# Performance work log

Measured on AMD Instinct MI355X. Metric: run time of the kernel, lower is better.

Reference implementation:

```python
import jax, jax.numpy as jnp
import numpy as np
import math

H, D = 8, 16
O = H * D  # out_channels = 128
N_TYPES = 2
EDGE_META = [(0, 1), (1, 0)]  # (src_type, dst_type) per edge type: user->item, item->user

def _segment_softmax(alpha, dst, n):
    # PyG softmax over incoming edges grouped by destination node
    amax = jax.ops.segment_max(alpha, dst, num_segments=n)
    amax = jnp.where(jnp.isfinite(amax), amax, 0.0)
    ex = jnp.exp(alpha - amax[dst])
    den = jax.ops.segment_sum(ex, dst, num_segments=n)
    return ex / (den[dst] + 1e-16)

def setup_inputs():
    key = jax.random.key(0)
    ks = jax.random.split(key, 8)
    N, E, I = 50000, 500000, 128
    s = 1.0 / math.sqrt(I)
    sd = 1.0 / math.sqrt(D)
    return {
        "x": jax.random.normal(ks[0], (N_TYPES, N, I), jnp.float32),
        "k_w": jax.random.normal(ks[1], (N_TYPES, O, I), jnp.float32) * s,
        "k_b": jnp.zeros((N_TYPES, O), jnp.float32),
        "q_w": jax.random.normal(ks[2], (N_TYPES, O, I), jnp.float32) * s,
        "q_b": jnp.zeros((N_TYPES, O), jnp.float32),
        "v_w": jax.random.normal(ks[3], (N_TYPES, O, I), jnp.float32) * s,
        "v_b": jnp.zeros((N_TYPES, O), jnp.float32),
        "a_w": jax.random.normal(ks[4], (N_TYPES, O, O), jnp.float32) * s,
        "a_b": jnp.zeros((N_TYPES, O), jnp.float32),
        "skip": jnp.ones((N_TYPES,), jnp.float32),
        "a_rel": jax.random.normal(ks[5], (2, H, D, D), jnp.float32) * sd,
        "m_rel": jax.random.normal(ks[6], (2, H, D, D), jnp.float32) * sd,
        "p_rel": jnp.ones((2, H), jnp.float32),
        "ln_g": jnp.ones((O,), jnp.float32),
        "ln_b": jnp.zeros((O,), jnp.float32),
        "edge_index": jax.random.randint(ks[7], (2, 2, E), 0, N, jnp.int32),
    }

def reference(x, k_w, k_b, q_w, q_b, v_w, v_b, a_w, a_b, skip, a_rel, m_rel, p_rel, ln_g, ln_b, edge_index):
    N = x.shape[1]
    lin = lambda xi, w, b: xi @ w.T + b
    # per-node-type K/Q/V projections -> [T, N, H, D]
    k = jnp.stack([lin(x[t], k_w[t], k_b[t]) for t in range(N_TYPES)]).reshape(N_TYPES, N, H, D)
    q = jnp.stack([lin(x[t], q_w[t], q_b[t]) for t in range(N_TYPES)]).reshape(N_TYPES, N, H, D)
    v = jnp.stack([lin(x[t], v_w[t], v_b[t]) for t in range(N_TYPES)]).reshape(N_TYPES, N, H, D)
    agg = jnp.zeros((N_TYPES, N, O), x.dtype)
    for e, (st, dt) in enumerate(EDGE_META):
        src, dst = edge_index[e, 0], edge_index[e, 1]
        ke = jnp.einsum('nhd,hde->nhe', k[st], a_rel[e])  # relation-transformed keys
        ve = jnp.einsum('nhd,hde->nhe', v[st], m_rel[e])  # relation-transformed values
        alpha = jnp.einsum('ehd,ehd->eh', q[dt][dst], ke[src]) * p_rel[e] / math.sqrt(D)
        alpha = _segment_softmax(alpha, dst, N)  # [E, H]
        msg = (ve[src] * alpha[..., None]).reshape(-1, O)
        agg = agg.at[dt].add(jax.ops.segment_sum(msg, dst, num_segments=N))
    outs = []
    for t in range(N_TYPES):
        o = lin(jax.nn.gelu(agg[t], approximate=False), a_w[t], a_b[t])
        beta = jax.nn.sigmoid(skip[t])
        o = beta * o + (1.0 - beta) * x[t]  # HGT skip (out_channels == in_channels)
        o = jax.nn.relu(o)
        mu = jnp.mean(o, axis=-1, keepdims=True)
        var = jnp.mean((o - mu) ** 2, axis=-1, keepdims=True)
        o = (o - mu) / jnp.sqrt(var + 1e-5) * ln_g + ln_b  # LayerNorm; dropout = identity (eval)
        outs.append(o)
    return jnp.stack(outs)  # [2, N, 128]
```

## Files before the change

### kernel.cpp

```cpp
#include <hip/hip_runtime.h>
#include <math.h>


#define EB_STRIDE 40

typedef __attribute__((ext_vector_type(8))) short short8;
typedef __attribute__((ext_vector_type(4))) float floatx4;

__device__ __forceinline__ float bf2f(unsigned int bits16) {
  union { unsigned int i; float f; } u; u.i = bits16 << 16; return u.f;
}
__device__ __forceinline__ unsigned short f2bf(float f) {
  union { float ff; unsigned int i; } u; u.ff = f;
  unsigned int x = u.i;
  x += 0x7fffu + ((x >> 16) & 1u);
  return (unsigned short)(x >> 16);
}

__global__ void fuse_weights(
    const float* __restrict__ k_w, const float* __restrict__ k_b,
    const float* __restrict__ q_w, const float* __restrict__ q_b,
    const float* __restrict__ v_w, const float* __restrict__ v_b,
    const float* __restrict__ a_w, const float* __restrict__ a_b,
    const float* __restrict__ a_rel, const float* __restrict__ m_rel,
    const float* __restrict__ p_rel,
    unsigned short* __restrict__ Wfb, float* __restrict__ Bf)
{
  int tid = blockIdx.x * 256 + threadIdx.x;
  if (tid >= 2 * 4 * 128 * 128) return;
  int t   = tid >> 16;
  int rem = tid & 65535;
  int m   = rem >> 14;
  int o   = (rem >> 7) & 127;
  int i   = rem & 127;
  float w, bias;
  if (m == 0) {
    w    = q_w[t * 16384 + o * 128 + i];
    bias = q_b[t * 128 + o];
  } else if (m == 3) {
    w    = a_w[t * 16384 + o * 128 + i];
    bias = a_b[t * 128 + o];
  } else {
    const float* bw  = (m == 1) ? k_w : v_w;
    const float* bb  = (m == 1) ? k_b : v_b;
    const float* rel = (m == 1) ? a_rel : m_rel;
    int h = o >> 4, eo = o & 15;
    float s = 0.f, sb = 0.f;
    #pragma unroll
    for (int d = 0; d < 16; ++d) {
      float r = rel[t * 2048 + h * 256 + d * 16 + eo];
      s  += bw[t * 16384 + (h * 16 + d) * 128 + i] * r;
      sb += bb[t * 128 + h * 16 + d] * r;
    }
    if (m == 1) {
      float sc = p_rel[t * 8 + h] * 0.25f;
      s *= sc; sb *= sc;
    }
    w = s; bias = sb;
  }
  Wfb[tid] = f2bf(w);
  if (i == 0) Bf[t * 512 + m * 128 + o] = bias;
}

__global__ void init_cnt(int* __restrict__ cnt, int nC)
{
  int tid = blockIdx.x * 256 + threadIdx.x;
  if (tid < nC) cnt[tid] = 0;
}

__global__ void fill_edges(const int* __restrict__ ei, int* __restrict__ cnt,
                           int* __restrict__ ebuf, int N, int E)
{
  int e = blockIdx.y;
  int i = blockIdx.x * 256 + threadIdx.x;
  if (i >= E) return;
  int src = ei[(size_t)e * 2 * E + i];
  int dst = ei[(size_t)e * 2 * E + E + i];
  int b = (1 - e) * N + dst;
  int pos = atomicAdd(&cnt[b], 1);
  if (pos < EB_STRIDE) ebuf[(size_t)b * EB_STRIDE + pos] = src;
}

__global__ __launch_bounds__(256) void gemm_qkv(
    const float* __restrict__ x, const unsigned short* __restrict__ Wfb,
    const float* __restrict__ Bf, unsigned short* __restrict__ qbuf,
    unsigned short* __restrict__ kvbuf, int Nn)
{
  __shared__ alignas(16) unsigned short Als[128][136];
  __shared__ alignas(16) unsigned short Bls[128][136];
  const int tid = threadIdx.x;
  const int t = blockIdx.y;
  const int m0 = blockIdx.x * 128;
  const int lane = tid & 63, w = tid >> 6;
  const int col = lane & 15, quad = lane >> 4;

  {
    int r = tid & 127, h = tid >> 7;
    int gn = m0 + r;
    if (gn < Nn) {
      const float* ap = x + (size_t)t * Nn * 128 + (size_t)gn * 128 + h * 64;
      #pragma unroll
      for (int j = 0; j < 16; ++j) {
        float4 f = ((const float4*)ap)[j];
        ushort4 s;
        s.x = f2bf(f.x); s.y = f2bf(f.y); s.z = f2bf(f.z); s.w = f2bf(f.w);
        *(ushort4*)&Als[r][h * 64 + j * 4] = s;
      }
    } else {
      ushort4 z = make_ushort4(0, 0, 0, 0);
      #pragma unroll
      for (int j = 0; j < 16; ++j) *(ushort4*)&Als[r][h * 64 + j * 4] = z;
    }
  }

  for (int m = 0; m < 3; ++m) {
    __syncthreads();
    {
      int r = tid & 127, h = tid >> 7;
      const unsigned short* wp = Wfb + (((size_t)(t * 4 + m)) << 14) + r * 128 + h * 64;
      #pragma unroll
      for (int j = 0; j < 8; ++j)
        *(uint4*)&Bls[r][h * 64 + j * 8] = ((const uint4*)wp)[j];
    }
    __syncthreads();

    floatx4 acc[2][8];
    #pragma unroll
    for (int mi = 0; mi < 2; ++mi)
      #pragma unroll
      for (int ni = 0; ni < 8; ++ni) acc[mi][ni] = (floatx4)(0.f);

    #pragma unroll
    for (int k0 = 0; k0 < 128; k0 += 32) {
      int kk = k0 + quad * 8;
      short8 a0 = *(const short8*)&Als[w * 32 + col][kk];
      short8 a1 = *(const short8*)&Als[w * 32 + 16 + col][kk];
      #pragma unroll
      for (int ni = 0; ni < 8; ++ni) {
        short8 b = *(const short8*)&Bls[ni * 16 + col][kk];
        acc[0][ni] = __builtin_amdgcn_mfma_f32_16x16x32_bf16(a0, b, acc[0][ni], 0, 0, 0);
        acc[1][ni] = __builtin_amdgcn_mfma_f32_16x16x32_bf16(a1, b, acc[1][ni], 0, 0, 0);
      }
    }

    const float* Bv = Bf + t * 512 + m * 128;
    float bias_n[8];
    #pragma unroll
    for (int ni = 0; ni < 8; ++ni) bias_n[ni] = Bv[ni * 16 + col];

    #pragma unroll
    for (int mi = 0; mi < 2; ++mi)
      #pragma unroll
      for (int reg = 0; reg < 4; ++reg) {
        int row = m0 + w * 32 + mi * 16 + quad * 4 + reg;
        if (row >= Nn) continue;
        if (m == 0) {
          unsigned short* cp = qbuf + ((size_t)t * Nn + row) * 128 + col;
          #pragma unroll
          for (int ni = 0; ni < 8; ++ni)
            cp[ni * 16] = f2bf(acc[mi][ni][reg] + bias_n[ni]);
        } else {
          unsigned short* cp = kvbuf + ((size_t)t * Nn + row) * 256 + 2 * col + (m - 1);
          #pragma unroll
          for (int ni = 0; ni < 8; ++ni)
            cp[ni * 32] = f2bf(acc[mi][ni][reg] + bias_n[ni]);
        }
      }
  }
}

__global__ __launch_bounds__(256) void gather_fused(
    const unsigned short* __restrict__ qbuf, const unsigned short* __restrict__ kvbuf,
    const int* __restrict__ cnt, const int* __restrict__ ebuf,
    unsigned short* __restrict__ gbuf, int N)
{
  int wid = (blockIdx.x * 256 + threadIdx.x) >> 6;
  int l = threadIdx.x & 63;
  if (wid >= 2 * N) return;
  int dt = (wid >= N) ? 1 : 0;
  int e  = 1 - dt;
  int deg = cnt[wid]; if (deg > EB_STRIDE) deg = EB_STRIDE;

  const unsigned short* qrow = qbuf + (size_t)wid * 128;
  float q0 = bf2f(qrow[l]);
  float q1 = bf2f(qrow[l + 64]);

  const unsigned short* kvbase = kvbuf + ((size_t)e * N) * 256;
  const int* eb = ebuf + (size_t)wid * EB_STRIDE;
  int mysrc = (l < deg) ? eb[l] : 0;

  float acc0 = 0.f, acc1 = 0.f, den0 = 0.f, den1 = 0.f;
  for (int j = 0; j < deg; ++j) {
    int src = __shfl(mysrc, j, 64);
    const unsigned short* kv = kvbase + (size_t)src * 256;
    unsigned int u0 = *(const unsigned int*)(kv + 2 * l);
    unsigned int u1 = *(const unsigned int*)(kv + 2 * l + 128);
    float p0 = q0 * bf2f(u0 & 0xffffu);
    float p1 = q1 * bf2f(u1 & 0xffffu);
    #pragma unroll
    for (int off = 1; off < 16; off <<= 1) {
      p0 += __shfl_xor(p0, off, 16);
      p1 += __shfl_xor(p1, off, 16);
    }
    float ex0 = __expf(p0);
    float ex1 = __expf(p1);
    acc0 = fmaf(ex0, bf2f(u0 >> 16), acc0); den0 += ex0;
    acc1 = fmaf(ex1, bf2f(u1 >> 16), acc1); den1 += ex1;
  }
  float g0 = acc0 / (den0 + 1e-16f);
  float g1 = acc1 / (den1 + 1e-16f);
  float r0 = 0.5f * g0 * (1.f + erff(g0 * 0.70710678118654752f));
  float r1 = 0.5f * g1 * (1.f + erff(g1 * 0.70710678118654752f));
  gbuf[(size_t)wid * 128 + l]      = f2bf(r0);
  gbuf[(size_t)wid * 128 + l + 64] = f2bf(r1);
}

__global__ __launch_bounds__(256) void gemm_ln(
    const unsigned short* __restrict__ gbuf, const unsigned short* __restrict__ Wfb,
    const float* __restrict__ Bf, const float* __restrict__ x,
    const float* __restrict__ skip, const float* __restrict__ ln_g,
    const float* __restrict__ ln_b, float* __restrict__ outp, int Nn)
{
  __shared__ alignas(16) unsigned short Als[128][136];
  __shared__ alignas(16) unsigned short Bls[128][136];
  const int tid = threadIdx.x;
  const int t = blockIdx.y;
  const int m0 = blockIdx.x * 128;
  const int lane = tid & 63, w = tid >> 6;
  const int col = lane & 15, quad = lane >> 4;

  {
    int r = tid & 127, h = tid >> 7;
    int gn = m0 + r;
    if (gn < Nn) {
      const unsigned short* ap = gbuf + (size_t)t * Nn * 128 + (size_t)gn * 128 + h * 64;
      #pragma unroll
      for (int j = 0; j < 8; ++j)
        *(uint4*)&Als[r][h * 64 + j * 8] = ((const uint4*)ap)[j];
    } else {
      uint4 z = make_uint4(0, 0, 0, 0);
      #pragma unroll
      for (int j = 0; j < 8; ++j) *(uint4*)&Als[r][h * 64 + j * 8] = z;
    }
  }
  {
    int r = tid & 127, h = tid >> 7;
    const unsigned short* wp = Wfb + (((size_t)(t * 4 + 3)) << 14) + r * 128 + h * 64;
    #pragma unroll
    for (int j = 0; j < 8; ++j)
      *(uint4*)&Bls[r][h * 64 + j * 8] = ((const uint4*)wp)[j];
  }
  __syncthreads();

  floatx4 acc[2][8];
  #pragma unroll
  for (int mi = 0; mi < 2; ++mi)
    #pragma unroll
    for (int ni = 0; ni < 8; ++ni) acc[mi][ni] = (floatx4)(0.f);

  #pragma unroll
  for (int k0 = 0; k0 < 128; k0 += 32) {
    int kk = k0 + quad * 8;
    short8 a0 = *(const short8*)&Als[w * 32 + col][kk];
    short8 a1 = *(const short8*)&Als[w * 32 + 16 + col][kk];
    #pragma unroll
    for (int ni = 0; ni < 8; ++ni) {
      short8 b = *(const short8*)&Bls[ni * 16 + col][kk];
      acc[0][ni] = __builtin_amdgcn_mfma_f32_16x16x32_bf16(a0, b, acc[0][ni], 0, 0, 0);
      acc[1][ni] = __builtin_amdgcn_mfma_f32_16x16x32_bf16(a1, b, acc[1][ni], 0, 0, 0);
    }
  }

  const float* Bv = Bf + t * 512 + 3 * 128;
  float bias_n[8], g_n[8], b_n[8];
  #pragma unroll
  for (int ni = 0; ni < 8; ++ni) {
    bias_n[ni] = Bv[ni * 16 + col];
    g_n[ni]    = ln_g[ni * 16 + col];
    b_n[ni]    = ln_b[ni * 16 + col];
  }
  float sv = skip[t];
  float beta = 1.f / (1.f + __expf(-sv));
  const float* xt = x + (size_t)t * Nn * 128;
  float* op = outp + (size_t)t * Nn * 128;

  #pragma unroll
  for (int mi = 0; mi < 2; ++mi)
    #pragma unroll
    for (int reg = 0; reg < 4; ++reg) {
      int row = m0 + w * 32 + mi * 16 + quad * 4 + reg;
      if (row >= Nn) continue;
      const float* xr = xt + (size_t)row * 128;
      float vals[8], s = 0.f;
      #pragma unroll
      for (int ni = 0; ni < 8; ++ni) {
        float o = acc[mi][ni][reg] + bias_n[ni];
        float v = fmaxf(beta * o + (1.f - beta) * xr[ni * 16 + col], 0.f);
        vals[ni] = v; s += v;
      }
      #pragma unroll
      for (int off = 1; off < 16; off <<= 1) s += __shfl_xor(s, off, 64);
      float mu = s * 0.0078125f;
      float sq = 0.f;
      #pragma unroll
      for (int ni = 0; ni < 8; ++ni) { float d = vals[ni] - mu; sq += d * d; }
      #pragma unroll
      for (int off = 1; off < 16; off <<= 1) sq += __shfl_xor(sq, off, 64);
      float rstd = rsqrtf(sq * 0.0078125f + 1e-5f);
      float* orow = op + (size_t)row * 128 + col;
      #pragma unroll
      for (int ni = 0; ni < 8; ++ni)
        orow[ni * 16] = (vals[ni] - mu) * rstd * g_n[ni] + b_n[ni];
    }
}

extern "C" void kernel_launch(void* const* d_in, const int* in_sizes, int n_in,
                              void* d_out, int out_size, void* d_ws, size_t ws_size,
                              hipStream_t stream) {
  const float* x     = (const float*)d_in[0];
  const float* k_w   = (const float*)d_in[1];
  const float* k_b   = (const float*)d_in[2];
  const float* q_w   = (const float*)d_in[3];
  const float* q_b   = (const float*)d_in[4];
  const float* v_w   = (const float*)d_in[5];
  const float* v_b   = (const float*)d_in[6];
  const float* a_w   = (const float*)d_in[7];
  const float* a_b   = (const float*)d_in[8];
  const float* skip  = (const float*)d_in[9];
  const float* a_rel = (const float*)d_in[10];
  const float* m_rel = (const float*)d_in[11];
  const float* p_rel = (const float*)d_in[12];
  const float* ln_g  = (const float*)d_in[13];
  const float* ln_b  = (const float*)d_in[14];
  const int* ei      = (const int*)d_in[15];
  float* out         = (float*)d_out;

  const int N = in_sizes[0] / 256;
  const int E = in_sizes[15] / 4;

  unsigned short* Wfb = (unsigned short*)d_ws;
  float* Bf = (float*)(Wfb + 2 * 4 * 128 * 128);
  unsigned short* qbuf = (unsigned short*)(Bf + 2 * 4 * 128);
  unsigned short* kvbuf = qbuf + (size_t)2 * N * 128;
  int* cnt  = (int*)(kvbuf + (size_t)2 * N * 256);
  int* ebuf = cnt + (size_t)2 * N;
  unsigned short* gbuf = (unsigned short*)(ebuf + (size_t)2 * N * EB_STRIDE);

  fuse_weights<<<(2 * 4 * 128 * 128 + 255) / 256, 256, 0, stream>>>(
      k_w, k_b, q_w, q_b, v_w, v_b, a_w, a_b, a_rel, m_rel, p_rel, Wfb, Bf);

  init_cnt<<<(2 * N + 255) / 256, 256, 0, stream>>>(cnt, 2 * N);

  fill_edges<<<dim3((E + 255) / 256, 2), 256, 0, stream>>>(ei, cnt, ebuf, N, E);

  int Mb = (N + 127) / 128;
  gemm_qkv<<<dim3(Mb, 2), 256, 0, stream>>>(x, Wfb, Bf, qbuf, kvbuf, N);

  gather_fused<<<(2 * N * 64 + 255) / 256, 256, 0, stream>>>(
      qbuf, kvbuf, cnt, ebuf, gbuf, N);

  gemm_ln<<<dim3(Mb, 2), 256, 0, stream>>>(
      gbuf, Wfb, Bf, x, skip, ln_g, ln_b, out, N);
}
```

Measured before the change: 370.0 us.

## Process four edges per wavefront in gather and read GEMM weights directly from global

The gather kernel now splits each 64-lane wavefront into four 16-lane groups. Each group handles a different incoming edge and each lane loads 16 contiguous bf16 K/V values with wide loads, so the per-edge shuffle reduction shrinks to a single xor. Partial sums are combined across groups with shuffles after the loop. Separately, both GEMM kernels drop the shared-memory B tile and read weight fragments straight from global/L2, which halves LDS use and removes barriers but makes the MFMA loop depend on global loads.

```diff
diff --git a/kernel.cpp b/kernel.cpp
--- a/kernel.cpp
+++ b/kernel.cpp
@@ -9,6 +9,9 @@
 
 __device__ __forceinline__ float bf2f(unsigned int bits16) {
   union { unsigned int i; float f; } u; u.i = bits16 << 16; return u.f;
+}
+__device__ __forceinline__ float bf2f_hi(unsigned int u) {
+  union { unsigned int i; float f; } v; v.i = u & 0xffff0000u; return v.f;
 }
 __device__ __forceinline__ unsigned short f2bf(float f) {
   union { float ff; unsigned int i; } u; u.ff = f;
@@ -87,7 +90,6 @@
     unsigned short* __restrict__ kvbuf, int Nn)
 {
   __shared__ alignas(16) unsigned short Als[128][136];
-  __shared__ alignas(16) unsigned short Bls[128][136];
   const int tid = threadIdx.x;
   const int t = blockIdx.y;
   const int m0 = blockIdx.x * 128;
@@ -112,17 +114,10 @@
       for (int j = 0; j < 16; ++j) *(ushort4*)&Als[r][h * 64 + j * 4] = z;
     }
   }
+  __syncthreads();
 
   for (int m = 0; m < 3; ++m) {
-    __syncthreads();
-    {
-      int r = tid & 127, h = tid >> 7;
-      const unsigned short* wp = Wfb + (((size_t)(t * 4 + m)) << 14) + r * 128 + h * 64;
-      #pragma unroll
-      for (int j = 0; j < 8; ++j)
-        *(uint4*)&Bls[r][h * 64 + j * 8] = ((const uint4*)wp)[j];
-    }
-    __syncthreads();
+    const unsigned short* Bm = Wfb + (((size_t)(t * 4 + m)) << 14);
 
     floatx4 acc[2][8];
     #pragma unroll
@@ -137,7 +132,7 @@
       short8 a1 = *(const short8*)&Als[w * 32 + 16 + col][kk];
       #pragma unroll
       for (int ni = 0; ni < 8; ++ni) {
-        short8 b = *(const short8*)&Bls[ni * 16 + col][kk];
+        short8 b = *(const short8*)(Bm + (size_t)(ni * 16 + col) * 128 + kk);
         acc[0][ni] = __builtin_amdgcn_mfma_f32_16x16x32_bf16(a0, b, acc[0][ni], 0, 0, 0);
         acc[1][ni] = __builtin_amdgcn_mfma_f32_16x16x32_bf16(a1, b, acc[1][ni], 0, 0, 0);
       }
@@ -180,39 +175,72 @@
   int dt = (wid >= N) ? 1 : 0;
   int e  = 1 - dt;
   int deg = cnt[wid]; if (deg > EB_STRIDE) deg = EB_STRIDE;
-
-  const unsigned short* qrow = qbuf + (size_t)wid * 128;
-  float q0 = bf2f(qrow[l]);
-  float q1 = bf2f(qrow[l + 64]);
+  int g = l >> 4, gl = l & 15;
+
+  uint4 qr = *(const uint4*)(qbuf + (size_t)wid * 128 + 8 * gl);
+  float qv[8];
+  qv[0] = bf2f(qr.x & 0xffffu); qv[1] = bf2f(qr.x >> 16);
+  qv[2] = bf2f(qr.y & 0xffffu); qv[3] = bf2f(qr.y >> 16);
+  qv[4] = bf2f(qr.z & 0xffffu); qv[5] = bf2f(qr.z >> 16);
+  qv[6] = bf2f(qr.w & 0xffffu); qv[7] = bf2f(qr.w >> 16);
 
   const unsigned short* kvbase = kvbuf + ((size_t)e * N) * 256;
   const int* eb = ebuf + (size_t)wid * EB_STRIDE;
   int mysrc = (l < deg) ? eb[l] : 0;
 
-  float acc0 = 0.f, acc1 = 0.f, den0 = 0.f, den1 = 0.f;
-  for (int j = 0; j < deg; ++j) {
-    int src = __shfl(mysrc, j, 64);
-    const unsigned short* kv = kvbase + (size_t)src * 256;
-    unsigned int u0 = *(const unsigned int*)(kv + 2 * l);
-    unsigned int u1 = *(const unsigned int*)(kv + 2 * l + 128);
-    float p0 = q0 * bf2f(u0 & 0xffffu);
-    float p1 = q1 * bf2f(u1 & 0xffffu);
-    #pragma unroll
-    for (int off = 1; off < 16; off <<= 1) {
-      p0 += __shfl_xor(p0, off, 16);
-      p1 += __shfl_xor(p1, off, 16);
-    }
-    float ex0 = __expf(p0);
-    float ex1 = __expf(p1);
-    acc0 = fmaf(ex0, bf2f(u0 >> 16), acc0); den0 += ex0;
-    acc1 = fmaf(ex1, bf2f(u1 >> 16), acc1); den1 += ex1;
-  }
-  float g0 = acc0 / (den0 + 1e-16f);
-  float g1 = acc1 / (den1 + 1e-16f);
-  float r0 = 0.5f * g0 * (1.f + erff(g0 * 0.70710678118654752f));
-  float r1 = 0.5f * g1 * (1.f + erff(g1 * 0.70710678118654752f));
-  gbuf[(size_t)wid * 128 + l]      = f2bf(r0);
-  gbuf[(size_t)wid * 128 + l + 64] = f2bf(r1);
+  float acc[8];
+  #pragma unroll
+  for (int c = 0; c < 8; ++c) acc[c] = 0.f;
+  float den = 0.f;
+
+  for (int j0 = 0; j0 < deg; j0 += 4) {
+    int j = j0 + g;
+    bool valid = j < deg;
+    int src = __shfl(mysrc, valid ? j : 0, 64);
+    const unsigned short* kv = kvbase + (size_t)src * 256 + 16 * gl;
+    uint4 a = *(const uint4*)kv;
+    uint4 b = *(const uint4*)(kv + 8);
+    float p;
+    p = qv[0] * bf2f(a.x & 0xffffu);
+    p = fmaf(qv[1], bf2f(a.y & 0xffffu), p);
+    p = fmaf(qv[2], bf2f(a.z & 0xffffu), p);
+    p = fmaf(qv[3], bf2f(a.w & 0xffffu), p);
+    p = fmaf(qv[4], bf2f(b.x & 0xffffu), p);
+    p = fmaf(qv[5], bf2f(b.y & 0xffffu), p);
+    p = fmaf(qv[6], bf2f(b.z & 0xffffu), p);
+    p = fmaf(qv[7], bf2f(b.w & 0xffffu), p);
+    float pt = p + __shfl_xor(p, 1, 64);
+    float ex = valid ? __expf(pt) : 0.f;
+    den += ex;
+    acc[0] = fmaf(ex, bf2f_hi(a.x), acc[0]);
+    acc[1] = fmaf(ex, bf2f_hi(a.y), acc[1]);
+    acc[2] = fmaf(ex, bf2f_hi(a.z), acc[2]);
+    acc[3] = fmaf(ex, bf2f_hi(a.w), acc[3]);
+    acc[4] = fmaf(ex, bf2f_hi(b.x), acc[4]);
+    acc[5] = fmaf(ex, bf2f_hi(b.y), acc[5]);
+    acc[6] = fmaf(ex, bf2f_hi(b.z), acc[6]);
+    acc[7] = fmaf(ex, bf2f_hi(b.w), acc[7]);
+  }
+
+  #pragma unroll
+  for (int off = 16; off < 64; off <<= 1) {
+    #pragma unroll
+    for (int c = 0; c < 8; ++c) acc[c] += __shfl_xor(acc[c], off, 64);
+    den += __shfl_xor(den, off, 64);
+  }
+
+  if (g == 0) {
+    float rden = 1.f / (den + 1e-16f);
+    unsigned short r[8];
+    #pragma unroll
+    for (int c = 0; c < 8; ++c) {
+      float gg = acc[c] * rden;
+      r[c] = f2bf(0.5f * gg * (1.f + erff(gg * 0.70710678118654752f)));
+    }
+    unsigned short* op = gbuf + (size_t)wid * 128 + 8 * gl;
+    *(ushort4*)op       = make_ushort4(r[0], r[1], r[2], r[3]);
+    *(ushort4*)(op + 4) = make_ushort4(r[4], r[5], r[6], r[7]);
+  }
 }
 
 __global__ __launch_bounds__(256) void gemm_ln(
@@ -222,7 +250,6 @@
     const float* __restrict__ ln_b, float* __restrict__ outp, int Nn)
 {
   __shared__ alignas(16) unsigned short Als[128][136];
-  __shared__ alignas(16) unsigned short Bls[128][136];
   const int tid = threadIdx.x;
   const int t = blockIdx.y;
   const int m0 = blockIdx.x * 128;
@@ -243,14 +270,9 @@
       for (int j = 0; j < 8; ++j) *(uint4*)&Als[r][h * 64 + j * 8] = z;
     }
   }
-  {
-    int r = tid & 127, h = tid >> 7;
-    const unsigned short* wp = Wfb + (((size_t)(t * 4 + 3)) << 14) + r * 128 + h * 64;
-    #pragma unroll
-    for (int j = 0; j < 8; ++j)
-      *(uint4*)&Bls[r][h * 64 + j * 8] = ((const uint4*)wp)[j];
-  }
   __syncthreads();
+
+  const unsigned short* Bm = Wfb + (((size_t)(t * 4 + 3)) << 14);
 
   floatx4 acc[2][8];
   #pragma unroll
@@ -265,7 +287,7 @@
     short8 a1 = *(const short8*)&Als[w * 32 + 16 + col][kk];
     #pragma unroll
     for (int ni = 0; ni < 8; ++ni) {
-      short8 b = *(const short8*)&Bls[ni * 16 + col][kk];
+      short8 b = *(const short8*)(Bm + (size_t)(ni * 16 + col) * 128 + kk);
       acc[0][ni] = __builtin_amdgcn_mfma_f32_16x16x32_bf16(a0, b, acc[0][ni], 0, 0, 0);
       acc[1][ni] = __builtin_amdgcn_mfma_f32_16x16x32_bf16(a1, b, acc[1][ni], 0, 0, 0);
     }
```

After: 375.0 us. No clear change (+1.3%).
